# Optimization experiments

Measured on AMD Instinct MI355X. Metric: run time of the kernel, lower is better.

Reference implementation:

```python
import jax, jax.numpy as jnp
import numpy as np

SITE, DIM = 8, 16
B = 8192
D = 2 * DIM

# --- static Z2-graded (Grassmann) bookkeeping -------------------------------
# Each edge (d, d) has parity 0 for the first d indices, parity 1 for the rest.
# Merging two graded edges reorders the flat product index so that all
# even-parity combinations come first (stable/lex within each sector).

def _merge_order(pA, pB):
    p = (pA[:, None] ^ pB[None, :]).reshape(-1)
    return np.argsort(p, kind='stable')

_P1 = np.array([0, 1])                                        # edge (1,1)
_PD = np.concatenate([np.zeros(DIM, np.int64), np.ones(DIM, np.int64)])  # edge (d,d)
ORDER_DD = _merge_order(_PD, _PD); INV_DD = np.argsort(ORDER_DD)
ORDER_1D = _merge_order(_P1, _PD); INV_1D = np.argsort(ORDER_1D)
ORDER_11 = _merge_order(_P1, _P1)                             # = [0,3,1,2]
MASK_X = jnp.asarray((_P1[:, None] ^ _PD[None, :]) == 0, jnp.float32)   # (2, D)
MASK_G2 = jnp.asarray((_PD[:, None] ^ _PD[None, :]) == 0, jnp.float32)  # (D, D)
MASK_G3 = jnp.asarray((_PD[:, None, None] ^ _PD[None, :, None] ^ _PD[None, None, :]) == 0, jnp.float32)
SIGN_PD = jnp.asarray(1.0 - 2.0 * _PD, jnp.float32)           # (-1)^parity, reverse sign
SWSIGN = jnp.asarray((-1.0) ** (_P1[:, None] * _PD[None, :]), jnp.float32)  # swap sign (2, D)


def setup_inputs() -> dict:
    key = jax.random.key(0)
    k1, k2, k3, k4 = jax.random.split(key, 4)
    return {
        'data': jax.random.randint(k1, (B, SITE), 0, 2),
        'embedding': jax.random.normal(k2, (SITE, 2, DIM), jnp.float32),
        'head_w': jax.random.normal(k3, (D, D), jnp.float32),
        'body_w': jax.random.normal(k4, (SITE - 1, D, D, D), jnp.float32),
    }


def _embed(emb_table, bits):
    # emb_table: (2, DIM); bits: (B,) in {0,1}
    emb = emb_table[bits]                                     # (B, DIM)
    zero = jnp.zeros_like(emb)
    on = bits[:, None] != 0
    row0 = jnp.concatenate([jnp.where(on, 0.0, emb), zero], -1)   # slot 0 (even,even)
    row1 = jnp.concatenate([zero, jnp.where(on, emb, 0.0)], -1)   # slot 3 (odd,odd)
    return jnp.stack([row0, row1], 1) * MASK_X                # (B, 2, D), even parity


def _body(x1, x2, g3):
    # x1, x2: (B, 2, D); g3: (D, D, D) with arrows (T, T, F)
    b = x1.shape[0]
    g = g3 * MASK_G3
    g = g * SIGN_PD[None, :, None]                            # reverse axis 1 (arrow flip)
    g_m = g.reshape(D, D * D)[:, ORDER_DD]                    # merge axes 1,2 even-first
    gx1 = jnp.einsum('bsk,km->bsm', x1 * MASK_X, g_m)         # (B, 2, D*D)
    gx1 = gx1[..., INV_DD].reshape(b, 2, D, D)                # split merged edge back
    gx1 = gx1 * SIGN_PD[None, None, :, None]                  # reverse axis 2
    gx1 = gx1 * SWSIGN[None, :, :, None]                      # graded sign: swap axes 1,2
    gx1_m = jnp.transpose(gx1, (0, 2, 1, 3)).reshape(b, D, 2 * D)[..., ORDER_1D]
    gx12 = jnp.einsum('bsk,bkm->bsm', x2 * MASK_X, gx1_m)     # (B, 2, 2D)
    gx12 = gx12[..., INV_1D].reshape(b, 2, 2, D)              # split into (s1 edge, (d,d))
    gx12 = gx12.reshape(b, 4, D)[:, ORDER_11, :]              # merge (s2, s1) even-first
    return gx12.reshape(b, 2, 2, D).sum(2)                    # sum per parity sector -> (B, 2, D)


def reference(data, embedding, head_w, body_w):
    x = _embed(embedding[0], data[:, 0])
    x = jnp.tanh(jnp.einsum('bsk,kj->bsj', x, head_w * MASK_G2))
    for i in range(1, SITE):
        x = jnp.tanh(_body(x, _embed(embedding[i], data[:, i]), body_w[i - 1]))
    return x
```

## Files before the change

kernel.cpp:

```cpp
#include <hip/hip_runtime.h>
#include <cmath>

#define SITE 8
#define DIM 16
#define BATCH 8192
#define NPAT 256

__global__ __launch_bounds__(256) void pattern_kernel(
    const float* __restrict__ embedding,
    const float* __restrict__ head_w,
    const float* __restrict__ body_w,
    float* __restrict__ pat)
{
    __shared__ float M[7][2][16][16];
    __shared__ float se[16], so[16];
    const int p = blockIdx.x;
    const int tid = threadIdx.x;

    #pragma unroll
    for (int r = 0; r < 14; ++r) {
        int t = tid + 256 * r;
        int s = t >> 9;
        int rem = t & 511;
        int h = rem >> 8;
        int e = rem & 255;
        int k = e >> 4;
        int j = e & 15;
        int bit = (p >> (s + 1)) & 1;
        const float* g3 = body_w + s * 32768;
        const float* emb = embedding + (s + 1) * 32 + bit * 16;
        float acc = 0.f;
        if (bit == 0) {
            if (h == 0) {
                #pragma unroll
                for (int i = 0; i < 16; ++i) acc += emb[i] * g3[k*1024 + i*32 + j];
            } else {
                #pragma unroll
                for (int i = 0; i < 16; ++i) acc += emb[i] * g3[(k+16)*1024 + i*32 + (j+16)];
            }
        } else {
            if (h == 0) {
                #pragma unroll
                for (int i = 0; i < 16; ++i) acc -= emb[i] * g3[(k+16)*1024 + (i+16)*32 + j];
            } else {
                #pragma unroll
                for (int i = 0; i < 16; ++i) acc += emb[i] * g3[k*1024 + (i+16)*32 + (j+16)];
            }
        }
        M[s][h][k][j] = acc;
    }

    if (tid < 32) {
        int h = tid >> 4;
        int j = tid & 15;
        int bit0 = p & 1;
        float v = 0.f;
        if (bit0 == 0 && h == 0) {
            const float* emb = embedding;
            float a = 0.f;
            #pragma unroll
            for (int k = 0; k < 16; ++k) a += emb[k] * head_w[k*32 + j];
            v = tanhf(a);
        } else if (bit0 == 1 && h == 1) {
            const float* emb = embedding + 16;
            float a = 0.f;
            #pragma unroll
            for (int k = 0; k < 16; ++k) a += emb[k] * head_w[(k+16)*32 + (j+16)];
            v = tanhf(a);
        }
        if (h == 0) se[j] = v; else so[j] = v;
    }
    __syncthreads();

    for (int s = 1; s < SITE; ++s) {
        float nv = 0.f;
        if (tid < 32) {
            int h = tid >> 4;
            int j = tid & 15;
            int bit = (p >> s) & 1;
            const float* src = (h == 0) ? (bit ? so : se) : (bit ? se : so);
            const float* m = &M[s-1][h][0][0];
            float a = 0.f;
            #pragma unroll
            for (int k = 0; k < 16; ++k) a += src[k] * m[k*16 + j];
            nv = tanhf(a);
        }
        __syncthreads();
        if (tid < 32) {
            int h = tid >> 4; int j = tid & 15;
            if (h == 0) se[j] = nv; else so[j] = nv;
        }
        __syncthreads();
    }

    if (tid < 32) {
        int h = tid >> 4; int j = tid & 15;
        pat[p * 32 + tid] = (h == 0) ? se[j] : so[j];
    }
}

__global__ __launch_bounds__(256) void scatter_kernel(
    const int* __restrict__ data,
    const float* __restrict__ pat,
    float* __restrict__ out)
{
    int gid = blockIdx.x * 256 + threadIdx.x;
    int b = gid >> 6;
    int t = gid & 63;
    if (b >= BATCH) return;
    const int* db = data + b * 8;
    int id = 0;
    #pragma unroll
    for (int i = 0; i < 8; ++i) id |= (db[i] & 1) << i;
    float v = 0.f;
    if (t < 16) v = pat[id * 32 + t];
    else if (t >= 48) v = pat[id * 32 + 16 + (t - 48)];
    out[b * 64 + t] = v;
}

extern "C" void kernel_launch(void* const* d_in, const int* in_sizes, int n_in,
                              void* d_out, int out_size, void* d_ws, size_t ws_size,
                              hipStream_t stream) {
    const int*   data      = (const int*)d_in[0];
    const float* embedding = (const float*)d_in[1];
    const float* head_w    = (const float*)d_in[2];
    const float* body_w    = (const float*)d_in[3];
    float* out = (float*)d_out;
    float* pat = (float*)d_ws;

    pattern_kernel<<<NPAT, 256, 0, stream>>>(embedding, head_w, body_w, pat);
    scatter_kernel<<<(BATCH * 64) / 256, 256, 0, stream>>>(data, pat, out);
}
```

Baseline: 72.75 us.

## Batch eight patterns per block and vectorize scatter with float4

Each pattern block now computes every per-site matrix for both bit values once and evaluates eight bit patterns in parallel, so 32 blocks replace 256 that each rebuilt the weight-contracted matrices and ran mostly idle 32-thread recurrences. The scatter kernel now reads data as int4 and writes output as float4, with a quarter as many threads. The aim is to remove redundant global-weight contractions and to cut memory instructions. In exchange, far fewer blocks occupy the GPU during the pattern stage.

```diff
diff --git a/kernel.cpp b/kernel.cpp
--- a/kernel.cpp
+++ b/kernel.cpp
@@ -12,110 +12,110 @@
     const float* __restrict__ body_w,
     float* __restrict__ pat)
 {
-    __shared__ float M[7][2][16][16];
-    __shared__ float se[16], so[16];
-    const int p = blockIdx.x;
+    __shared__ float M[7][2][2][256];
+    __shared__ float hv[2][16];
+    __shared__ float st[8][2][16];
+
     const int tid = threadIdx.x;
+    const int pbase = blockIdx.x * 8;
 
-    #pragma unroll
-    for (int r = 0; r < 14; ++r) {
-        int t = tid + 256 * r;
-        int s = t >> 9;
-        int rem = t & 511;
-        int h = rem >> 8;
-        int e = rem & 255;
-        int k = e >> 4;
-        int j = e & 15;
-        int bit = (p >> (s + 1)) & 1;
-        const float* g3 = body_w + s * 32768;
-        const float* emb = embedding + (s + 1) * 32 + bit * 16;
-        float acc = 0.f;
-        if (bit == 0) {
-            if (h == 0) {
-                #pragma unroll
-                for (int i = 0; i < 16; ++i) acc += emb[i] * g3[k*1024 + i*32 + j];
+    {
+        const int k = tid >> 4;
+        const int j = tid & 15;
+        for (int r = 0; r < 28; ++r) {
+            int s   = r >> 2;
+            int bit = (r >> 1) & 1;
+            int h   = r & 1;
+            const float* g3  = body_w + s * 32768;
+            const float* emb = embedding + (s + 1) * 32 + bit * 16;
+            float acc = 0.f;
+            if (bit == 0) {
+                if (h == 0) {
+                    #pragma unroll
+                    for (int i = 0; i < 16; ++i) acc += emb[i] * g3[k*1024 + i*32 + j];
+                } else {
+                    #pragma unroll
+                    for (int i = 0; i < 16; ++i) acc += emb[i] * g3[(k+16)*1024 + i*32 + (j+16)];
+                }
             } else {
-                #pragma unroll
-                for (int i = 0; i < 16; ++i) acc += emb[i] * g3[(k+16)*1024 + i*32 + (j+16)];
+                if (h == 0) {
+                    #pragma unroll
+                    for (int i = 0; i < 16; ++i) acc -= emb[i] * g3[(k+16)*1024 + (i+16)*32 + j];
+                } else {
+                    #pragma unroll
+                    for (int i = 0; i < 16; ++i) acc += emb[i] * g3[k*1024 + (i+16)*32 + (j+16)];
+                }
             }
-        } else {
-            if (h == 0) {
-                #pragma unroll
-                for (int i = 0; i < 16; ++i) acc -= emb[i] * g3[(k+16)*1024 + (i+16)*32 + j];
-            } else {
-                #pragma unroll
-                for (int i = 0; i < 16; ++i) acc += emb[i] * g3[k*1024 + (i+16)*32 + (j+16)];
-            }
+            M[s][bit][h][tid & 255] = acc;
         }
-        M[s][h][k][j] = acc;
     }
 
     if (tid < 32) {
         int h = tid >> 4;
         int j = tid & 15;
-        int bit0 = p & 1;
-        float v = 0.f;
-        if (bit0 == 0 && h == 0) {
-            const float* emb = embedding;
-            float a = 0.f;
+        const float* emb = embedding + h * 16;
+        float a = 0.f;
+        if (h == 0) {
             #pragma unroll
             for (int k = 0; k < 16; ++k) a += emb[k] * head_w[k*32 + j];
-            v = tanhf(a);
-        } else if (bit0 == 1 && h == 1) {
-            const float* emb = embedding + 16;
-            float a = 0.f;
+        } else {
             #pragma unroll
             for (int k = 0; k < 16; ++k) a += emb[k] * head_w[(k+16)*32 + (j+16)];
-            v = tanhf(a);
         }
-        if (h == 0) se[j] = v; else so[j] = v;
+        hv[h][j] = tanhf(a);
+    }
+    __syncthreads();
+
+    {
+        int pl = tid >> 5;
+        int h  = (tid >> 4) & 1;
+        int j  = tid & 15;
+        int bit0 = (pbase + pl) & 1;
+        st[pl][h][j] = (h == bit0) ? hv[h][j] : 0.f;
     }
     __syncthreads();
 
     for (int s = 1; s < SITE; ++s) {
-        float nv = 0.f;
-        if (tid < 32) {
-            int h = tid >> 4;
-            int j = tid & 15;
-            int bit = (p >> s) & 1;
-            const float* src = (h == 0) ? (bit ? so : se) : (bit ? se : so);
-            const float* m = &M[s-1][h][0][0];
-            float a = 0.f;
-            #pragma unroll
-            for (int k = 0; k < 16; ++k) a += src[k] * m[k*16 + j];
-            nv = tanhf(a);
-        }
+        int pl = tid >> 5;
+        int h  = (tid >> 4) & 1;
+        int j  = tid & 15;
+        int bit = ((pbase + pl) >> s) & 1;
+        const float* src = st[pl][h ^ bit];
+        const float* m   = &M[s-1][bit][h][0];
+        float a = 0.f;
+        #pragma unroll
+        for (int k = 0; k < 16; ++k) a += src[k] * m[k*16 + j];
+        float nv = tanhf(a);
         __syncthreads();
-        if (tid < 32) {
-            int h = tid >> 4; int j = tid & 15;
-            if (h == 0) se[j] = nv; else so[j] = nv;
-        }
+        st[pl][h][j] = nv;
         __syncthreads();
     }
 
-    if (tid < 32) {
-        int h = tid >> 4; int j = tid & 15;
-        pat[p * 32 + tid] = (h == 0) ? se[j] : so[j];
+    {
+        int pl = tid >> 5;
+        int h  = (tid >> 4) & 1;
+        int j  = tid & 15;
+        pat[(pbase + pl) * 32 + h * 16 + j] = st[pl][h][j];
     }
 }
 
 __global__ __launch_bounds__(256) void scatter_kernel(
     const int* __restrict__ data,
-    const float* __restrict__ pat,
-    float* __restrict__ out)
+    const float4* __restrict__ pat4,
+    float4* __restrict__ out4)
 {
     int gid = blockIdx.x * 256 + threadIdx.x;
-    int b = gid >> 6;
-    int t = gid & 63;
-    if (b >= BATCH) return;
-    const int* db = data + b * 8;
-    int id = 0;
-    #pragma unroll
-    for (int i = 0; i < 8; ++i) id |= (db[i] & 1) << i;
-    float v = 0.f;
-    if (t < 16) v = pat[id * 32 + t];
-    else if (t >= 48) v = pat[id * 32 + 16 + (t - 48)];
-    out[b * 64 + t] = v;
+    int b = gid >> 4;
+    int q = gid & 15;
+    const int4* d4 = (const int4*)(data + b * 8);
+    int4 w0 = d4[0];
+    int4 w1 = d4[1];
+    int id = (w0.x & 1) | ((w0.y & 1) << 1) | ((w0.z & 1) << 2) | ((w0.w & 1) << 3)
+           | ((w1.x & 1) << 4) | ((w1.y & 1) << 5) | ((w1.z & 1) << 6) | ((w1.w & 1) << 7);
+    float4 v = make_float4(0.f, 0.f, 0.f, 0.f);
+    if (q < 4)       v = pat4[id * 8 + q];
+    else if (q >= 12) v = pat4[id * 8 + (q - 8)];
+    out4[b * 16 + q] = v;
 }
 
 extern "C" void kernel_launch(void* const* d_in, const int* in_sizes, int n_in,
@@ -125,9 +125,9 @@
     const float* embedding = (const float*)d_in[1];
     const float* head_w    = (const float*)d_in[2];
     const float* body_w    = (const float*)d_in[3];
-    float* out = (float*)d_out;
     float* pat = (float*)d_ws;
 
-    pattern_kernel<<<NPAT, 256, 0, stream>>>(embedding, head_w, body_w, pat);
-    scatter_kernel<<<(BATCH * 64) / 256, 256, 0, stream>>>(data, pat, out);
+    pattern_kernel<<<32, 256, 0, stream>>>(embedding, head_w, body_w, pat);
+    scatter_kernel<<<(BATCH * 16) / 256, 256, 0, stream>>>(data, (const float4*)pat,
+                                                           (float4*)d_out);
 }
```

Result: slower. 78.51 us (+7.9%).
